# Kernel tuning notes

Measured on AMD Instinct MI355X. Metric: run time of the kernel, lower is better.

Reference implementation:

```python
import jax, jax.numpy as jnp
import numpy as np

B, N, C = 64, 1024, 128
H1, H2 = 256, 128
ACTION = N


def _xavier(key, shape):
    lim = float(np.sqrt(6.0 / (shape[0] + shape[1])))
    return jax.random.uniform(key, shape, jnp.float32, -lim, lim)


def setup_inputs() -> dict:
    key = jax.random.key(0)
    ks = jax.random.split(key, 16)
    node_features = jax.random.normal(ks[0], (B, N, 3), jnp.float32)
    adjacency_matrix = jax.random.randint(ks[1], (B, N, N), 0, 2).astype(jnp.int32)
    return {
        "node_features": node_features,
        "adjacency_matrix": adjacency_matrix,
        "W_in": _xavier(ks[2], (3, C)),
        "a_src": _xavier(ks[3], (C, 1)),
        "a_dst": _xavier(ks[4], (C, 1)),
        "a_src2": _xavier(ks[5], (C, 1)),
        "a_dst2": _xavier(ks[6], (C, 1)),
        "W1": _xavier(ks[7], (C, H1)),
        "b1": jnp.zeros((H1,), jnp.float32),
        "W2": _xavier(ks[8], (H1, H2)),
        "b2": jnp.zeros((H2,), jnp.float32),
        "Wpi": _xavier(ks[9], (H2, ACTION)),
        "bpi": jnp.zeros((ACTION,), jnp.float32),
        "Wv": _xavier(ks[10], (H2, 1)),
        "bv": jnp.zeros((1,), jnp.float32),
    }


def _gat_layer(x, mask, a_src, a_dst):
    # x: [B,N,C]; mask: [B,N,N] bool
    ai = jnp.squeeze(x @ a_src, -1)  # [B,N] score of node as source (i)
    aj = jnp.squeeze(x @ a_dst, -1)  # [B,N] score of node as dest (j)
    e = ai[:, :, None] + aj[:, None, :]  # [B,N,N]
    e = jnp.where(e > 0, e, 0.2 * e)  # leaky_relu(0.2)
    e = jnp.where(mask, e, jnp.float32(-1e9))  # masked_fill(-inf)
    alpha = jax.nn.softmax(e, axis=-1)  # [B,N,N]
    out = jnp.einsum("bij,bjc->bic", alpha, x)  # weighted neighbor aggregation
    return jax.nn.relu(out)


def reference(node_features, adjacency_matrix, W_in, a_src, a_dst, a_src2, a_dst2,
              W1, b1, W2, b2, Wpi, bpi, Wv, bv):
    mask = adjacency_matrix > 0
    x = node_features @ W_in  # [B,N,C], no bias
    x = _gat_layer(x, mask, a_src, a_dst)
    x = _gat_layer(x, mask, a_src2, a_dst2)
    x = jnp.mean(x, axis=1)  # [B,C]
    x = jax.nn.relu(x @ W1 + b1)
    x = jax.nn.relu(x @ W2 + b2)
    pi = jax.nn.softmax(x @ Wpi + bpi, axis=1)
    v = x @ Wv + bv
    return (pi, v)
```

## Files before the change

### kernel.cpp

```cpp
#include <hip/hip_runtime.h>

#define Bn 64
#define Nn 1024
#define Cc 128

typedef _Float16 h8 __attribute__((ext_vector_type(8)));
typedef float f4v __attribute__((ext_vector_type(4)));
typedef unsigned long long u64;

__global__ __launch_bounds__(256) void k_feat(
    const float* __restrict__ nf, const float* __restrict__ Win,
    const float* __restrict__ asrc, const float* __restrict__ adst,
    _Float16* __restrict__ X0, float* __restrict__ ai, float* __restrict__ aj,
    float* __restrict__ E, float* __restrict__ G, float* __restrict__ F, float* __restrict__ H) {
  int g = blockIdx.x; int b = g >> 7; int n0 = (g & 127) << 3;
  int t = threadIdx.x; int c = t >> 1; int h = t & 1;
  float w0 = Win[c], w1 = Win[Cc + c], w2 = Win[2 * Cc + c];
  float as_ = asrc[c], ad = adst[c];
  float ps[4], pd[4];
  _Float16 hv[4];
  #pragma unroll
  for (int r = 0; r < 4; r++) {
    int n = n0 + (h << 2) + r;
    const float* p = nf + ((size_t)(b << 10) + n) * 3;
    float x = p[0] * w0 + p[1] * w1 + p[2] * w2;
    hv[r] = (_Float16)x; ps[r] = x * as_; pd[r] = x * ad;
  }
  *(uint2*)(X0 + ((size_t)b << 17) + ((size_t)(g & 127) << 10) + (c << 3) + (h << 2)) = *(uint2*)hv;
  #pragma unroll
  for (int off = 32; off > 1; off >>= 1) {
    #pragma unroll
    for (int r = 0; r < 4; r++) { ps[r] += __shfl_down(ps[r], off, 64); pd[r] += __shfl_down(pd[r], off, 64); }
  }
  __shared__ float red[4][2][4][2];
  int lane = t & 63, wv = t >> 6;
  if (lane < 2) {
    #pragma unroll
    for (int r = 0; r < 4; r++) { red[wv][lane][r][0] = ps[r]; red[wv][lane][r][1] = pd[r]; }
  }
  __syncthreads();
  if (t < 8) {
    int hh = t >> 2, r = t & 3;
    float sa = 0.f, sd = 0.f;
    #pragma unroll
    for (int w = 0; w < 4; w++) { sa += red[w][hh][r][0]; sd += red[w][hh][r][1]; }
    int gi = (b << 10) + n0 + t;
    ai[gi] = sa; aj[gi] = sd;
    E[gi] = __expf(sa); G[gi] = __expf(0.2f * sa);
    F[gi] = __expf(sd); H[gi] = __expf(0.2f * sd);
  }
}

__global__ __launch_bounds__(256) void k_scores2(
    const _Float16* __restrict__ X1,
    const float* __restrict__ asrc, const float* __restrict__ adst,
    float* __restrict__ ai, float* __restrict__ aj,
    float* __restrict__ E, float* __restrict__ G, float* __restrict__ F, float* __restrict__ H) {
  int g = blockIdx.x; int b = g >> 7; int n0 = (g & 127) << 3;
  int t = threadIdx.x; int c = t >> 1; int h = t & 1;
  float as_ = asrc[c], ad = adst[c];
  uint2 raw = *(const uint2*)(X1 + ((size_t)b << 17) + ((size_t)(g & 127) << 10) + (c << 3) + (h << 2));
  const _Float16* hp = (const _Float16*)&raw;
  float ps[4], pd[4];
  #pragma unroll
  for (int r = 0; r < 4; r++) { float x = (float)hp[r]; ps[r] = x * as_; pd[r] = x * ad; }
  #pragma unroll
  for (int off = 32; off > 1; off >>= 1) {
    #pragma unroll
    for (int r = 0; r < 4; r++) { ps[r] += __shfl_down(ps[r], off, 64); pd[r] += __shfl_down(pd[r], off, 64); }
  }
  __shared__ float red[4][2][4][2];
  int lane = t & 63, wv = t >> 6;
  if (lane < 2) {
    #pragma unroll
    for (int r = 0; r < 4; r++) { red[wv][lane][r][0] = ps[r]; red[wv][lane][r][1] = pd[r]; }
  }
  __syncthreads();
  if (t < 8) {
    int hh = t >> 2, r = t & 3;
    float sa = 0.f, sd = 0.f;
    #pragma unroll
    for (int w = 0; w < 4; w++) { sa += red[w][hh][r][0]; sd += red[w][hh][r][1]; }
    int gi = (b << 10) + n0 + t;
    ai[gi] = sa; aj[gi] = sd;
    E[gi] = __expf(sa); G[gi] = __expf(0.2f * sa);
    F[gi] = __expf(sd); H[gi] = __expf(0.2f * sd);
  }
}

template <int LAYER>
__global__ __launch_bounds__(256, 3) void k_agg(
    const _Float16* __restrict__ X, const int* __restrict__ adj,
    const float* __restrict__ ai, const float* __restrict__ E, const float* __restrict__ G,
    const float* __restrict__ aj, const float* __restrict__ F, const float* __restrict__ H,
    u64* __restrict__ pm, _Float16* __restrict__ Y, float* __restrict__ xmp) {
  __shared__ __align__(16) char smem[33792];
  float* s_aj = (float*)smem;
  float* s_F  = (float*)(smem + 4096);
  float* s_H  = (float*)(smem + 8192);
  unsigned char* s_pm = (unsigned char*)(smem + 12288);
  float* tile = (float*)smem;

  const int b = blockIdx.y, i0 = blockIdx.x << 6;
  const int tid = threadIdx.x;
  const int lane = tid & 63, wv = tid >> 6;
  const int m = lane & 15, quad = lane >> 4;
  const int wi = wv >> 1, wc = wv & 1;
  const int gbase = b << 10;

  ((float4*)s_aj)[tid] = ((const float4*)(aj + gbase))[tid];
  ((float4*)s_F)[tid]  = ((const float4*)(F + gbase))[tid];
  ((float4*)s_H)[tid]  = ((const float4*)(H + gbase))[tid];

  if (LAYER == 1) {
    ushort* pmu = (ushort*)pm;
    #pragma unroll 2
    for (int pass = 0; pass < 16; ++pass) {
      int r = (wv << 4) + pass;
      const uint4* arow = (const uint4*)(adj + ((size_t)(gbase + i0 + r) << 10));
      uint4 v0 = arow[(lane << 2) | 0], v1 = arow[(lane << 2) | 1];
      uint4 v2 = arow[(lane << 2) | 2], v3 = arow[(lane << 2) | 3];
      unsigned int bits =
          (v0.x) | (v0.y << 1) | (v0.z << 2) | (v0.w << 3) |
          (v1.x << 4) | (v1.y << 5) | (v1.z << 6) | (v1.w << 7) |
          (v2.x << 8) | (v2.y << 9) | (v2.z << 10) | (v2.w << 11) |
          (v3.x << 12) | (v3.y << 13) | (v3.z << 14) | (v3.w << 15);
      *(ushort*)(s_pm + r * 152 + (lane << 1)) = (ushort)bits;
      pmu[((size_t)(gbase + i0 + r) << 6) + lane] = (ushort)bits;
    }
  } else {
    const u64* pmg = pm + (((size_t)(gbase + i0)) << 4);
    #pragma unroll
    for (int k = tid; k < 1024; k += 256) {
      int r = k >> 4, w = k & 15;
      *(u64*)(s_pm + r * 152 + (w << 3)) = pmg[k];
    }
  }

  const int r0 = (wi << 5) + m;
  const int gi0 = gbase + i0 + r0;
  const float ai0 = ai[gi0],      E0c = E[gi0],      G0c = G[gi0];
  const float ai1 = ai[gi0 + 16], E1c = E[gi0 + 16], G1c = G[gi0 + 16];
  float dsum0 = 0.f, dsum1 = 0.f;

  f4v acc[2][4];
  #pragma unroll
  for (int a = 0; a < 2; a++)
    #pragma unroll
    for (int ct = 0; ct < 4; ct++) { f4v z = {0.f, 0.f, 0.f, 0.f}; acc[a][ct] = z; }

  const char* gB = (const char*)(X + ((size_t)b << 17)) + (((quad << 7) + (wc << 6) + m) << 4);
  const unsigned char* pmr0 = s_pm + r0 * 152;
  const unsigned char* pmr1 = pmr0 + 16 * 152;

  __syncthreads();

  for (int kt = 0; kt < 32; ++kt) {
    h8 b0 = *(const h8*)(gB);
    h8 b1 = *(const h8*)(gB + 256);
    h8 b2 = *(const h8*)(gB + 512);
    h8 b3 = *(const h8*)(gB + 768);
    gB += 8192;
    const int j0 = (kt << 5) + (quad << 3);
    float aw[8], fw[8], hw[8];
    *(float4*)&aw[0] = *(const float4*)&s_aj[j0]; *(float4*)&aw[4] = *(const float4*)&s_aj[j0 + 4];
    *(float4*)&fw[0] = *(const float4*)&s_F[j0];  *(float4*)&fw[4] = *(const float4*)&s_F[j0 + 4];
    *(float4*)&hw[0] = *(const float4*)&s_H[j0];  *(float4*)&hw[4] = *(const float4*)&s_H[j0 + 4];
    unsigned int mb0 = pmr0[(kt << 2) + quad];
    unsigned int mb1 = pmr1[(kt << 2) + quad];
    h8 a0, a1;
    #pragma unroll
    for (int e = 0; e < 8; e++) {
      float ew = aw[e], fe = fw[e], he = hw[e];
      bool p0 = (ai0 + ew) > 0.f;
      float v0 = (p0 ? E0c : G0c) * (p0 ? fe : he);
      v0 = ((mb0 >> e) & 1u) ? v0 : 0.f;
      dsum0 += v0; a0[e] = (_Float16)v0;
      bool p1 = (ai1 + ew) > 0.f;
      float v1 = (p1 ? E1c : G1c) * (p1 ? fe : he);
      v1 = ((mb1 >> e) & 1u) ? v1 : 0.f;
      dsum1 += v1; a1[e] = (_Float16)v1;
    }
    acc[0][0] = __builtin_amdgcn_mfma_f32_16x16x32_f16(a0, b0, acc[0][0], 0, 0, 0);
    acc[1][0] = __builtin_amdgcn_mfma_f32_16x16x32_f16(a1, b0, acc[1][0], 0, 0, 0);
    acc[0][1] = __builtin_amdgcn_mfma_f32_16x16x32_f16(a0, b1, acc[0][1], 0, 0, 0);
    acc[1][1] = __builtin_amdgcn_mfma_f32_16x16x32_f16(a1, b1, acc[1][1], 0, 0, 0);
    acc[0][2] = __builtin_amdgcn_mfma_f32_16x16x32_f16(a0, b2, acc[0][2], 0, 0, 0);
    acc[1][2] = __builtin_amdgcn_mfma_f32_16x16x32_f16(a1, b2, acc[1][2], 0, 0, 0);
    acc[0][3] = __builtin_amdgcn_mfma_f32_16x16x32_f16(a0, b3, acc[0][3], 0, 0, 0);
    acc[1][3] = __builtin_amdgcn_mfma_f32_16x16x32_f16(a1, b3, acc[1][3], 0, 0, 0);
  }

  dsum0 += __shfl_xor(dsum0, 16, 64);
  dsum0 += __shfl_xor(dsum0, 32, 64);
  dsum1 += __shfl_xor(dsum1, 16, 64);
  dsum1 += __shfl_xor(dsum1, 32, 64);
  float rd8[2][4];
  #pragma unroll
  for (int r = 0; r < 4; r++) {
    int src = (quad << 2) + r;
    rd8[0][r] = 1.0f / __shfl(dsum0, src, 64);
    rd8[1][r] = 1.0f / __shfl(dsum1, src, 64);
  }

  __syncthreads();
  #pragma unroll
  for (int a = 0; a < 2; a++)
    #pragma unroll
    for (int ct = 0; ct < 4; ct++)
      #pragma unroll
      for (int r = 0; r < 4; r++) {
        int lr = (wi << 5) + (a << 4) + (quad << 2) + r;
        int c = (wc << 6) + (ct << 4) + m;
        tile[lr * 132 + c] = fmaxf(acc[a][ct][r] * rd8[a][r], 0.f);
      }
  __syncthreads();
  if (LAYER == 1) {
    _Float16 hv[32];
    #pragma unroll
    for (int s = 0; s < 32; s++) {
      int q = (tid << 5) + s;
      int li = ((q >> 10) << 3) + (q & 7), c = (q >> 3) & 127;
      hv[s] = (_Float16)tile[li * 132 + c];
    }
    uint4* o = (uint4*)(Y + ((size_t)b << 17) + ((size_t)i0 << 7) + (tid << 5));
    o[0] = *(uint4*)&hv[0]; o[1] = *(uint4*)&hv[8];
    o[2] = *(uint4*)&hv[16]; o[3] = *(uint4*)&hv[24];
  } else {
    if (tid < 128) {
      float s = 0.f;
      #pragma unroll
      for (int i = 0; i < 64; i++) s += tile[i * 132 + tid];
      xmp[(((b << 4) + blockIdx.x) << 7) + tid] = s;
    }
  }
}

__global__ __launch_bounds__(256) void k_head(
    const float* __restrict__ xmp, const float* __restrict__ W1, const float* __restrict__ b1,
    const float* __restrict__ W2, const float* __restrict__ b2,
    const float* __restrict__ Wpi, const float* __restrict__ bpi,
    const float* __restrict__ Wv, const float* __restrict__ bv,
    float* __restrict__ out) {
  int b = blockIdx.x, t = threadIdx.x;
  __shared__ float xs[128], h1[256], h2[128], red[4];
  if (t < 128) {
    const float* p = xmp + ((size_t)b << 11);
    float s = 0.f;
    #pragma unroll
    for (int xb = 0; xb < 16; xb++) s += p[(xb << 7) + t];
    xs[t] = s * (1.f / 1024.f);
  }
  __syncthreads();
  float s = 0.f;
  #pragma unroll 8
  for (int k = 0; k < 128; k++) s += xs[k] * W1[k * 256 + t];
  h1[t] = fmaxf(s + b1[t], 0.f);
  __syncthreads();
  if (t < 128) {
    float s2 = 0.f;
    #pragma unroll 8
    for (int k = 0; k < 256; k++) s2 += h1[k] * W2[k * 128 + t];
    h2[t] = fmaxf(s2 + b2[t], 0.f);
  }
  __syncthreads();
  float lg[4];
  #pragma unroll
  for (int q = 0; q < 4; q++) {
    int o = t + (q << 8);
    float s3 = 0.f;
    #pragma unroll 8
    for (int k = 0; k < 128; k++) s3 += h2[k] * Wpi[k * 1024 + o];
    lg[q] = s3 + bpi[o];
  }
  float mx = fmaxf(fmaxf(lg[0], lg[1]), fmaxf(lg[2], lg[3]));
  #pragma unroll
  for (int off = 32; off > 0; off >>= 1) mx = fmaxf(mx, __shfl_down(mx, off, 64));
  if ((t & 63) == 0) red[t >> 6] = mx;
  __syncthreads();
  mx = fmaxf(fmaxf(red[0], red[1]), fmaxf(red[2], red[3]));
  __syncthreads();
  float ex[4]; float sum = 0.f;
  #pragma unroll
  for (int q = 0; q < 4; q++) { ex[q] = __expf(lg[q] - mx); sum += ex[q]; }
  #pragma unroll
  for (int off = 32; off > 0; off >>= 1) sum += __shfl_down(sum, off, 64);
  if ((t & 63) == 0) red[t >> 6] = sum;
  __syncthreads();
  sum = red[0] + red[1] + red[2] + red[3];
  float rs = 1.0f / sum;
  #pragma unroll
  for (int q = 0; q < 4; q++) out[((size_t)b << 10) + t + (q << 8)] = ex[q] * rs;
  __syncthreads();
  float vp = (t < 128) ? h2[t] * Wv[t] : 0.f;
  #pragma unroll
  for (int off = 32; off > 0; off >>= 1) vp += __shfl_down(vp, off, 64);
  if ((t & 63) == 0) red[t >> 6] = vp;
  __syncthreads();
  if (t == 0) out[65536 + b] = red[0] + red[1] + red[2] + red[3] + bv[0];
}

extern "C" void kernel_launch(void* const* d_in, const int* in_sizes, int n_in,
                              void* d_out, int out_size, void* d_ws, size_t ws_size,
                              hipStream_t stream) {
  const float* nf    = (const float*)d_in[0];
  const int*   adj   = (const int*)  d_in[1];
  const float* Win   = (const float*)d_in[2];
  const float* asrc  = (const float*)d_in[3];
  const float* adst  = (const float*)d_in[4];
  const float* asrc2 = (const float*)d_in[5];
  const float* adst2 = (const float*)d_in[6];
  const float* W1    = (const float*)d_in[7];
  const float* b1    = (const float*)d_in[8];
  const float* W2    = (const float*)d_in[9];
  const float* b2    = (const float*)d_in[10];
  const float* Wpi   = (const float*)d_in[11];
  const float* bpi   = (const float*)d_in[12];
  const float* Wv    = (const float*)d_in[13];
  const float* bv    = (const float*)d_in[14];
  float* out = (float*)d_out;

  char* ws = (char*)d_ws;
  _Float16* x0 = (_Float16*)(ws);
  _Float16* x1 = (_Float16*)(ws + 16777216);
  u64* pm = (u64*)(ws + 33554432);
  char* S = ws + 41943040;
  float* ai1 = (float*)(S + 0 * 262144);
  float* aj1 = (float*)(S + 1 * 262144);
  float* E1  = (float*)(S + 2 * 262144);
  float* G1  = (float*)(S + 3 * 262144);
  float* F1  = (float*)(S + 4 * 262144);
  float* H1  = (float*)(S + 5 * 262144);
  float* ai2 = (float*)(S + 6 * 262144);
  float* aj2 = (float*)(S + 7 * 262144);
  float* E2  = (float*)(S + 8 * 262144);
  float* G2  = (float*)(S + 9 * 262144);
  float* F2  = (float*)(S + 10 * 262144);
  float* H2  = (float*)(S + 11 * 262144);
  float* xmp = (float*)(S + 12 * 262144);

  k_feat<<<8192, 256, 0, stream>>>(nf, Win, asrc, adst, x0, ai1, aj1, E1, G1, F1, H1);
  dim3 ag(16, Bn);
  k_agg<1><<<ag, 256, 0, stream>>>(x0, adj, ai1, E1, G1, aj1, F1, H1, pm, x1, nullptr);
  k_scores2<<<8192, 256, 0, stream>>>(x1, asrc2, adst2, ai2, aj2, E2, G2, F2, H2);
  k_agg<2><<<ag, 256, 0, stream>>>(x1, nullptr, ai2, E2, G2, aj2, F2, H2, pm, nullptr, xmp);
  k_head<<<Bn, 256, 0, stream>>>(xmp, W1, b1, W2, b2, Wpi, bpi, Wv, bv, out);
}
```

Measured before the change: 573.4 us.

## Fuse layer-2 score computation into layer-1 aggregation and double-buffer k-loop

Removes the separate layer-2 score kernel by computing source/destination attention scores and their exponentials in the layer-1 aggregation epilogue from the fp32 output tile. The aggregation k-loop is software-pipelined with two register buffer sets so loads of the next step overlap compute. The grid is linearised with batch as the fastest index, and k_feat stages node features in shared memory. This trades extra registers (possible occupancy loss) and slight numeric differences for one fewer launch and less global traffic.

```diff
diff --git a/kernel.cpp b/kernel.cpp
--- a/kernel.cpp
+++ b/kernel.cpp
@@ -15,14 +15,16 @@
     float* __restrict__ E, float* __restrict__ G, float* __restrict__ F, float* __restrict__ H) {
   int g = blockIdx.x; int b = g >> 7; int n0 = (g & 127) << 3;
   int t = threadIdx.x; int c = t >> 1; int h = t & 1;
+  __shared__ float sNf[24];
+  if (t < 24) sNf[t] = nf[((size_t)(b << 10) + n0) * 3 + t];
   float w0 = Win[c], w1 = Win[Cc + c], w2 = Win[2 * Cc + c];
   float as_ = asrc[c], ad = adst[c];
+  __syncthreads();
   float ps[4], pd[4];
   _Float16 hv[4];
   #pragma unroll
   for (int r = 0; r < 4; r++) {
-    int n = n0 + (h << 2) + r;
-    const float* p = nf + ((size_t)(b << 10) + n) * 3;
+    const float* p = sNf + ((h << 2) + r) * 3;
     float x = p[0] * w0 + p[1] * w1 + p[2] * w2;
     hv[r] = (_Float16)x; ps[r] = x * as_; pd[r] = x * ad;
   }
@@ -51,57 +53,27 @@
   }
 }
 
-__global__ __launch_bounds__(256) void k_scores2(
-    const _Float16* __restrict__ X1,
-    const float* __restrict__ asrc, const float* __restrict__ adst,
-    float* __restrict__ ai, float* __restrict__ aj,
-    float* __restrict__ E, float* __restrict__ G, float* __restrict__ F, float* __restrict__ H) {
-  int g = blockIdx.x; int b = g >> 7; int n0 = (g & 127) << 3;
-  int t = threadIdx.x; int c = t >> 1; int h = t & 1;
-  float as_ = asrc[c], ad = adst[c];
-  uint2 raw = *(const uint2*)(X1 + ((size_t)b << 17) + ((size_t)(g & 127) << 10) + (c << 3) + (h << 2));
-  const _Float16* hp = (const _Float16*)&raw;
-  float ps[4], pd[4];
-  #pragma unroll
-  for (int r = 0; r < 4; r++) { float x = (float)hp[r]; ps[r] = x * as_; pd[r] = x * ad; }
-  #pragma unroll
-  for (int off = 32; off > 1; off >>= 1) {
-    #pragma unroll
-    for (int r = 0; r < 4; r++) { ps[r] += __shfl_down(ps[r], off, 64); pd[r] += __shfl_down(pd[r], off, 64); }
-  }
-  __shared__ float red[4][2][4][2];
-  int lane = t & 63, wv = t >> 6;
-  if (lane < 2) {
-    #pragma unroll
-    for (int r = 0; r < 4; r++) { red[wv][lane][r][0] = ps[r]; red[wv][lane][r][1] = pd[r]; }
-  }
-  __syncthreads();
-  if (t < 8) {
-    int hh = t >> 2, r = t & 3;
-    float sa = 0.f, sd = 0.f;
-    #pragma unroll
-    for (int w = 0; w < 4; w++) { sa += red[w][hh][r][0]; sd += red[w][hh][r][1]; }
-    int gi = (b << 10) + n0 + t;
-    ai[gi] = sa; aj[gi] = sd;
-    E[gi] = __expf(sa); G[gi] = __expf(0.2f * sa);
-    F[gi] = __expf(sd); H[gi] = __expf(0.2f * sd);
-  }
-}
-
 template <int LAYER>
 __global__ __launch_bounds__(256, 3) void k_agg(
     const _Float16* __restrict__ X, const int* __restrict__ adj,
     const float* __restrict__ ai, const float* __restrict__ E, const float* __restrict__ G,
     const float* __restrict__ aj, const float* __restrict__ F, const float* __restrict__ H,
-    u64* __restrict__ pm, _Float16* __restrict__ Y, float* __restrict__ xmp) {
-  __shared__ __align__(16) char smem[33792];
+    u64* __restrict__ pm, _Float16* __restrict__ Y, float* __restrict__ xmp,
+    const float* __restrict__ as2, const float* __restrict__ ad2,
+    float* __restrict__ ai2o, float* __restrict__ aj2o,
+    float* __restrict__ E2o, float* __restrict__ G2o,
+    float* __restrict__ F2o, float* __restrict__ H2o) {
+  __shared__ __align__(16) char smem[34816];
   float* s_aj = (float*)smem;
   float* s_F  = (float*)(smem + 4096);
   float* s_H  = (float*)(smem + 8192);
   unsigned char* s_pm = (unsigned char*)(smem + 12288);
   float* tile = (float*)smem;
-
-  const int b = blockIdx.y, i0 = blockIdx.x << 6;
+  float* s_as2 = (float*)(smem + 33792);
+  float* s_ad2 = (float*)(smem + 34304);
+
+  const int lin = blockIdx.x;
+  const int b = lin & 63, tile_id = lin >> 6, i0 = tile_id << 6;
   const int tid = threadIdx.x;
   const int lane = tid & 63, wv = tid >> 6;
   const int m = lane & 15, quad = lane >> 4;
@@ -111,6 +83,7 @@
   ((float4*)s_aj)[tid] = ((const float4*)(aj + gbase))[tid];
   ((float4*)s_F)[tid]  = ((const float4*)(F + gbase))[tid];
   ((float4*)s_H)[tid]  = ((const float4*)(H + gbase))[tid];
+  if (LAYER == 1 && tid < 128) { s_as2[tid] = as2[tid]; s_ad2[tid] = ad2[tid]; }
 
   if (LAYER == 1) {
     ushort* pmu = (ushort*)pm;
@@ -153,42 +126,58 @@
   const unsigned char* pmr0 = s_pm + r0 * 152;
   const unsigned char* pmr1 = pmr0 + 16 * 152;
 
-  __syncthreads();
-
-  for (int kt = 0; kt < 32; ++kt) {
-    h8 b0 = *(const h8*)(gB);
-    h8 b1 = *(const h8*)(gB + 256);
-    h8 b2 = *(const h8*)(gB + 512);
-    h8 b3 = *(const h8*)(gB + 768);
-    gB += 8192;
+  auto LOADK = [&](int kt, h8& B0, h8& B1, h8& B2, h8& B3,
+                   float4& W0, float4& W1, float4& Fw0, float4& Fw1,
+                   float4& Hw0, float4& Hw1, unsigned& M0, unsigned& M1) {
+    const char* gp = gB + ((size_t)kt << 13);
+    B0 = *(const h8*)gp;          B1 = *(const h8*)(gp + 256);
+    B2 = *(const h8*)(gp + 512);  B3 = *(const h8*)(gp + 768);
     const int j0 = (kt << 5) + (quad << 3);
+    W0  = *(const float4*)&s_aj[j0]; W1  = *(const float4*)&s_aj[j0 + 4];
+    Fw0 = *(const float4*)&s_F[j0];  Fw1 = *(const float4*)&s_F[j0 + 4];
+    Hw0 = *(const float4*)&s_H[j0];  Hw1 = *(const float4*)&s_H[j0 + 4];
+    M0 = pmr0[(kt << 2) + quad];     M1 = pmr1[(kt << 2) + quad];
+  };
+  auto COMP = [&](h8 B0, h8 B1, h8 B2, h8 B3,
+                  float4 W0, float4 W1, float4 Fw0, float4 Fw1,
+                  float4 Hw0, float4 Hw1, unsigned M0, unsigned M1) {
     float aw[8], fw[8], hw[8];
-    *(float4*)&aw[0] = *(const float4*)&s_aj[j0]; *(float4*)&aw[4] = *(const float4*)&s_aj[j0 + 4];
-    *(float4*)&fw[0] = *(const float4*)&s_F[j0];  *(float4*)&fw[4] = *(const float4*)&s_F[j0 + 4];
-    *(float4*)&hw[0] = *(const float4*)&s_H[j0];  *(float4*)&hw[4] = *(const float4*)&s_H[j0 + 4];
-    unsigned int mb0 = pmr0[(kt << 2) + quad];
-    unsigned int mb1 = pmr1[(kt << 2) + quad];
+    *(float4*)&aw[0] = W0;  *(float4*)&aw[4] = W1;
+    *(float4*)&fw[0] = Fw0; *(float4*)&fw[4] = Fw1;
+    *(float4*)&hw[0] = Hw0; *(float4*)&hw[4] = Hw1;
     h8 a0, a1;
     #pragma unroll
     for (int e = 0; e < 8; e++) {
       float ew = aw[e], fe = fw[e], he = hw[e];
       bool p0 = (ai0 + ew) > 0.f;
       float v0 = (p0 ? E0c : G0c) * (p0 ? fe : he);
-      v0 = ((mb0 >> e) & 1u) ? v0 : 0.f;
+      v0 = ((M0 >> e) & 1u) ? v0 : 0.f;
       dsum0 += v0; a0[e] = (_Float16)v0;
       bool p1 = (ai1 + ew) > 0.f;
       float v1 = (p1 ? E1c : G1c) * (p1 ? fe : he);
-      v1 = ((mb1 >> e) & 1u) ? v1 : 0.f;
+      v1 = ((M1 >> e) & 1u) ? v1 : 0.f;
       dsum1 += v1; a1[e] = (_Float16)v1;
     }
-    acc[0][0] = __builtin_amdgcn_mfma_f32_16x16x32_f16(a0, b0, acc[0][0], 0, 0, 0);
-    acc[1][0] = __builtin_amdgcn_mfma_f32_16x16x32_f16(a1, b0, acc[1][0], 0, 0, 0);
-    acc[0][1] = __builtin_amdgcn_mfma_f32_16x16x32_f16(a0, b1, acc[0][1], 0, 0, 0);
-    acc[1][1] = __builtin_amdgcn_mfma_f32_16x16x32_f16(a1, b1, acc[1][1], 0, 0, 0);
-    acc[0][2] = __builtin_amdgcn_mfma_f32_16x16x32_f16(a0, b2, acc[0][2], 0, 0, 0);
-    acc[1][2] = __builtin_amdgcn_mfma_f32_16x16x32_f16(a1, b2, acc[1][2], 0, 0, 0);
-    acc[0][3] = __builtin_amdgcn_mfma_f32_16x16x32_f16(a0, b3, acc[0][3], 0, 0, 0);
-    acc[1][3] = __builtin_amdgcn_mfma_f32_16x16x32_f16(a1, b3, acc[1][3], 0, 0, 0);
+    acc[0][0] = __builtin_amdgcn_mfma_f32_16x16x32_f16(a0, B0, acc[0][0], 0, 0, 0);
+    acc[1][0] = __builtin_amdgcn_mfma_f32_16x16x32_f16(a1, B0, acc[1][0], 0, 0, 0);
+    acc[0][1] = __builtin_amdgcn_mfma_f32_16x16x32_f16(a0, B1, acc[0][1], 0, 0, 0);
+    acc[1][1] = __builtin_amdgcn_mfma_f32_16x16x32_f16(a1, B1, acc[1][1], 0, 0, 0);
+    acc[0][2] = __builtin_amdgcn_mfma_f32_16x16x32_f16(a0, B2, acc[0][2], 0, 0, 0);
+    acc[1][2] = __builtin_amdgcn_mfma_f32_16x16x32_f16(a1, B2, acc[1][2], 0, 0, 0);
+    acc[0][3] = __builtin_amdgcn_mfma_f32_16x16x32_f16(a0, B3, acc[0][3], 0, 0, 0);
+    acc[1][3] = __builtin_amdgcn_mfma_f32_16x16x32_f16(a1, B3, acc[1][3], 0, 0, 0);
+  };
+
+  __syncthreads();
+
+  h8 Ab0, Ab1, Ab2, Ab3; float4 Aw0, Aw1, Af0, Af1, Ah0, Ah1; unsigned Am0, Am1;
+  h8 Bb0, Bb1, Bb2, Bb3; float4 Bw0, Bw1, Bf0, Bf1, Bh0, Bh1; unsigned Bm0, Bm1;
+  LOADK(0, Ab0, Ab1, Ab2, Ab3, Aw0, Aw1, Af0, Af1, Ah0, Ah1, Am0, Am1);
+  for (int kt = 0; kt < 32; kt += 2) {
+    LOADK(kt + 1, Bb0, Bb1, Bb2, Bb3, Bw0, Bw1, Bf0, Bf1, Bh0, Bh1, Bm0, Bm1);
+    COMP(Ab0, Ab1, Ab2, Ab3, Aw0, Aw1, Af0, Af1, Ah0, Ah1, Am0, Am1);
+    LOADK(kt + 2, Ab0, Ab1, Ab2, Ab3, Aw0, Aw1, Af0, Af1, Ah0, Ah1, Am0, Am1);
+    COMP(Bb0, Bb1, Bb2, Bb3, Bw0, Bw1, Bf0, Bf1, Bh0, Bh1, Bm0, Bm1);
   }
 
   dsum0 += __shfl_xor(dsum0, 16, 64);
@@ -226,12 +215,30 @@
     uint4* o = (uint4*)(Y + ((size_t)b << 17) + ((size_t)i0 << 7) + (tid << 5));
     o[0] = *(uint4*)&hv[0]; o[1] = *(uint4*)&hv[8];
     o[2] = *(uint4*)&hv[16]; o[3] = *(uint4*)&hv[24];
+    {
+      int i = tid >> 2, p = tid & 3, cb = p << 5;
+      const float* trow = tile + i * 132 + cb;
+      float ssrc = 0.f, sdst = 0.f;
+      #pragma unroll
+      for (int k = 0; k < 32; k += 4) {
+        float4 tv = *(const float4*)(trow + k);
+        float4 av = *(const float4*)(s_as2 + cb + k);
+        float4 dv = *(const float4*)(s_ad2 + cb + k);
+        ssrc += tv.x * av.x + tv.y * av.y + tv.z * av.z + tv.w * av.w;
+        sdst += tv.x * dv.x + tv.y * dv.y + tv.z * dv.z + tv.w * dv.w;
+      }
+      ssrc += __shfl_xor(ssrc, 1, 64); ssrc += __shfl_xor(ssrc, 2, 64);
+      sdst += __shfl_xor(sdst, 1, 64); sdst += __shfl_xor(sdst, 2, 64);
+      int gi = gbase + i0 + i;
+      if (p == 0) { ai2o[gi] = ssrc; E2o[gi] = __expf(ssrc); G2o[gi] = __expf(0.2f * ssrc); }
+      else if (p == 1) { aj2o[gi] = sdst; F2o[gi] = __expf(sdst); H2o[gi] = __expf(0.2f * sdst); }
+    }
   } else {
     if (tid < 128) {
       float s = 0.f;
       #pragma unroll
       for (int i = 0; i < 64; i++) s += tile[i * 132 + tid];
-      xmp[(((b << 4) + blockIdx.x) << 7) + tid] = s;
+      xmp[(((b << 4) + tile_id) << 7) + tid] = s;
     }
   }
 }
@@ -340,9 +347,9 @@
   float* xmp = (float*)(S + 12 * 262144);
 
   k_feat<<<8192, 256, 0, stream>>>(nf, Win, asrc, adst, x0, ai1, aj1, E1, G1, F1, H1);
-  dim3 ag(16, Bn);
-  k_agg<1><<<ag, 256, 0, stream>>>(x0, adj, ai1, E1, G1, aj1, F1, H1, pm, x1, nullptr);
-  k_scores2<<<8192, 256, 0, stream>>>(x1, asrc2, adst2, ai2, aj2, E2, G2, F2, H2);
-  k_agg<2><<<ag, 256, 0, stream>>>(x1, nullptr, ai2, E2, G2, aj2, F2, H2, pm, nullptr, xmp);
+  k_agg<1><<<1024, 256, 0, stream>>>(x0, adj, ai1, E1, G1, aj1, F1, H1, pm, x1, nullptr,
+                                     asrc2, adst2, ai2, aj2, E2, G2, F2, H2);
+  k_agg<2><<<1024, 256, 0, stream>>>(x1, nullptr, ai2, E2, G2, aj2, F2, H2, pm, nullptr, xmp,
+                                     nullptr, nullptr, nullptr, nullptr, nullptr, nullptr, nullptr, nullptr);
   k_head<<<Bn, 256, 0, stream>>>(xmp, W1, b1, W2, b2, Wpi, bpi, Wv, bv, out);
 }
```

Measured after the change: 564.6 us. Within noise of the previous version (-1.5%).
